# Kernel optimization log

Hardware: AMD Instinct MI355X
Metric: run time of the kernel (lower is better)

The kernel has to match this reference:

```python
import jax, jax.numpy as jnp
import numpy as np

B, S, D = 2, 2048, 512
H, DK, DV = 8, 64, 64
TEMP = DK ** 0.5


def setup_inputs() -> dict:
    key = jax.random.key(0)
    ks = jax.random.split(key, 12)
    inp = {
        "q": jax.random.normal(ks[0], (B, S, D), dtype=jnp.float32),
        "k": jax.random.normal(ks[1], (B, S, D), dtype=jnp.float32),
        "v": jax.random.normal(ks[2], (B, S, D), dtype=jnp.float32),
        "static_cov": jax.random.normal(ks[3], (B, S, S), dtype=jnp.float32),
        "mask": jax.random.randint(ks[4], (B, S, S), 0, 2, dtype=jnp.int32),
        # learned params (torch Linear(bias=False) weight is [out,in]; we store [in,out])
        "w_q": jax.random.normal(ks[5], (D, H * DK), dtype=jnp.float32) / np.sqrt(D),
        "w_k": jax.random.normal(ks[6], (D, H * DK), dtype=jnp.float32) / np.sqrt(D),
        "w_v": jax.random.normal(ks[7], (D, H * DV), dtype=jnp.float32) / np.sqrt(D),
        "w_fc": jax.random.normal(ks[8], (H * DV, D), dtype=jnp.float32) / np.sqrt(H * DV),
        "lambda_w": 10.0 * jnp.ones((1, H, 1, 1), dtype=jnp.float32),
        "ln_gamma": jnp.ones((D,), dtype=jnp.float32),
        "ln_beta": jnp.zeros((D,), dtype=jnp.float32),
    }
    return inp


def reference(q, k, v, static_cov, mask, w_q, w_k, w_v, w_fc, lambda_w, ln_gamma, ln_beta):
    residual = q
    # LayerNorm(eps=1e-6) on q only
    mu = jnp.mean(q, axis=-1, keepdims=True)
    var = jnp.mean(jnp.square(q - mu), axis=-1, keepdims=True)
    qn = (q - mu) / jnp.sqrt(var + 1e-6) * ln_gamma + ln_beta
    # projections -> [B, H, S, d]
    qh = (qn @ w_q).reshape(B, S, H, DK).transpose(0, 2, 1, 3)
    kh = (k @ w_k).reshape(B, S, H, DK).transpose(0, 2, 1, 3)
    vh = (v @ w_v).reshape(B, S, H, DV).transpose(0, 2, 1, 3)
    # convex blend of QK^T and static bias
    scores = jnp.einsum('bhqd,bhkd->bhqk', qh / TEMP, kh)  # [B,H,S,S]
    attn = scores / (lambda_w + 1.0) + (lambda_w / (lambda_w + 1.0)) * static_cov[:, None]
    attn = jnp.where(mask[:, None] == 0, -1e9, attn)
    attn = jax.nn.softmax(attn, axis=-1)
    out = jnp.einsum('bhqk,bhkd->bhqd', attn, vh)
    out = out.transpose(0, 2, 1, 3).reshape(B, S, H * DV)
    out = out @ w_fc + residual
    return (out, attn)
```

## Files before the change

### kernel.cpp

```cpp
#include <hip/hip_runtime.h>
#include <hip/hip_bf16.h>

typedef __attribute__((ext_vector_type(4))) float f32x4;
typedef __attribute__((ext_vector_type(4))) int i32x4;
typedef __attribute__((ext_vector_type(4))) unsigned int u32x4;
typedef __attribute__((ext_vector_type(8))) __bf16 bf16x8;

#define SDIM 2048
#define DDIM 512
#define HH 8
#define DH 64

static __device__ __forceinline__ f32x4 mfma_raw(bf16x8 a, bf16x8 b, f32x4 c) {
  return __builtin_amdgcn_mfma_f32_16x16x32_bf16(a, b, c, 0, 0, 0);
}

template <bool C1>
static __device__ __forceinline__ f32x4 mf(bf16x8 a, bf16x8 b, f32x4 c) {
  return C1 ? mfma_raw(a, b, c) : mfma_raw(b, a, c);
}

static __device__ __forceinline__ unsigned pack_bf16(float a, float b) {
  __bf16 x = (__bf16)a, y = (__bf16)b;
  unsigned short ux = __builtin_bit_cast(unsigned short, x);
  unsigned short uy = __builtin_bit_cast(unsigned short, y);
  return ((unsigned)uy << 16) | (unsigned)ux;
}

__global__ __launch_bounds__(256) void stageA_kernel(const float* __restrict__ cov,
                                                     const int* __restrict__ mask,
                                                     float* __restrict__ covm,
                                                     const float* __restrict__ q,
                                                     const float* __restrict__ gamma,
                                                     const float* __restrict__ beta,
                                                     __bf16* __restrict__ qn,
                                                     const float* __restrict__ w0,
                                                     const float* __restrict__ w1,
                                                     const float* __restrict__ w2,
                                                     const float* __restrict__ w3,
                                                     __bf16* __restrict__ t0,
                                                     __bf16* __restrict__ t1,
                                                     __bf16* __restrict__ t2,
                                                     __bf16* __restrict__ t3,
                                                     int* __restrict__ flag) {
  __shared__ float tile[64][65];
  int bid = blockIdx.x;
  if (bid < 8192) {
    size_t i = ((size_t)bid * 256 + threadIdx.x) * 4;
    f32x4 c = *(const f32x4*)(cov + i);
    i32x4 m = *(const i32x4*)(mask + i);
    f32x4 o;
#pragma unroll
    for (int r = 0; r < 4; ++r) o[r] = (m[r] == 0) ? -1e38f : c[r];
    *(f32x4*)(covm + i) = o;
    return;
  }
  if (bid < 9216) {
    int lb = bid - 8192;
    if (lb == 0 && threadIdx.x < 64) {
      float av = (float)(threadIdx.x & 15);
      float bv = av * av;
      bf16x8 a, b;
#pragma unroll
      for (int i = 0; i < 8; ++i) { a[i] = (__bf16)av; b[i] = (__bf16)bv; }
      f32x4 d = {};
      d = mfma_raw(a, b, d);
      if (threadIdx.x == 17) *flag = (d[0] == 128.0f) ? 1 : 2;
    }
    int row = lb * 4 + (threadIdx.x >> 6);
    int lane = threadIdx.x & 63;
    const float* qr = q + (size_t)row * DDIM + lane * 8;
    f32x4 x0 = *(const f32x4*)qr;
    f32x4 x1 = *(const f32x4*)(qr + 4);
    float s = 0.f;
#pragma unroll
    for (int i = 0; i < 4; ++i) s += x0[i] + x1[i];
#pragma unroll
    for (int off = 32; off; off >>= 1) s += __shfl_xor(s, off);
    float mu = s * (1.f / DDIM);
    float vs = 0.f;
#pragma unroll
    for (int i = 0; i < 4; ++i) {
      float d0 = x0[i] - mu, d1 = x1[i] - mu;
      vs += d0 * d0 + d1 * d1;
    }
#pragma unroll
    for (int off = 32; off; off >>= 1) vs += __shfl_xor(vs, off);
    float inv = rsqrtf(vs * (1.f / DDIM) + 1e-6f);
    const float* g = gamma + lane * 8;
    const float* be = beta + lane * 8;
    bf16x8 o;
#pragma unroll
    for (int i = 0; i < 8; ++i) {
      float xv = (i < 4) ? x0[i] : x1[i - 4];
      o[i] = (__bf16)((xv - mu) * inv * g[i] + be[i]);
    }
    *(bf16x8*)(qn + (size_t)row * DDIM + lane * 8) = o;
    return;
  }
  int wb = bid - 9216;
  int which = wb >> 6;
  int rem = wb & 63;
  int n0 = (rem & 7) * 64;
  int k0 = (rem >> 3) * 64;
  const float* w = which == 0 ? w0 : which == 1 ? w1 : which == 2 ? w2 : w3;
  __bf16* t = which == 0 ? t0 : which == 1 ? t1 : which == 2 ? t2 : t3;
  int tx = threadIdx.x & 63, ty = threadIdx.x >> 6;
#pragma unroll
  for (int j = 0; j < 16; ++j) {
    int kk = ty * 16 + j;
    tile[kk][tx] = w[(size_t)(k0 + kk) * DDIM + n0 + tx];
  }
  __syncthreads();
#pragma unroll
  for (int j = 0; j < 16; ++j) {
    int n = ty * 16 + j;
    t[(size_t)(n0 + n) * DDIM + k0 + tx] = (__bf16)tile[tx][n];
  }
}

template <bool C1>
static __device__ __forceinline__ void proj_body(const __bf16* __restrict__ qn,
                                                 const float* __restrict__ kin,
                                                 const float* __restrict__ vin,
                                                 const __bf16* __restrict__ wqT,
                                                 const __bf16* __restrict__ wkT,
                                                 const __bf16* __restrict__ wvT,
                                                 const float* __restrict__ lam,
                                                 __bf16* __restrict__ qh,
                                                 __bf16* __restrict__ kh,
                                                 __bf16* __restrict__ vT,
                                                 __bf16* __restrict__ tr) {
  int which = blockIdx.z;
  int n0 = blockIdx.x * 64;
  int m0 = blockIdx.y * 64;
  int wid = threadIdx.x >> 6, lane = threadIdx.x & 63;
  int lr = lane & 15, lg = lane >> 4;
  int mrow = m0 + wid * 16;
  const __bf16* wT = which == 0 ? wqT : which == 1 ? wkT : wvT;
  f32x4 acc[4] = {};
  for (int kb = 0; kb < DDIM; kb += 32) {
    bf16x8 afrag;
    if (which == 0) {
      afrag = *(const bf16x8*)(qn + (size_t)(mrow + lr) * DDIM + kb + lg * 8);
    } else {
      const float* src = (which == 1 ? kin : vin) + (size_t)(mrow + lr) * DDIM + kb + lg * 8;
      f32x4 y0 = *(const f32x4*)src;
      f32x4 y1 = *(const f32x4*)(src + 4);
#pragma unroll
      for (int i = 0; i < 4; ++i) { afrag[i] = (__bf16)y0[i]; afrag[i + 4] = (__bf16)y1[i]; }
    }
#pragma unroll
    for (int c = 0; c < 4; ++c) {
      bf16x8 bfrag = *(const bf16x8*)(wT + (size_t)(n0 + c * 16 + lr) * DDIM + kb + lg * 8);
      acc[c] = mf<C1>(afrag, bfrag, acc[c]);
    }
  }
  int h = n0 >> 6;
  int bq = m0 >> 11;
  int ss0 = m0 & 2047;
  if (which == 0) {
    float sc = 1.f / (8.f * (lam[h] + 1.f));
#pragma unroll
    for (int c = 0; c < 4; ++c)
#pragma unroll
      for (int r = 0; r < 4; ++r)
        tr[(wid * 16 + lg * 4 + r) * 72 + c * 16 + lr] = (__bf16)(acc[c][r] * sc);
  } else if (which == 1) {
#pragma unroll
    for (int c = 0; c < 4; ++c)
#pragma unroll
      for (int r = 0; r < 4; ++r)
        tr[(wid * 16 + lg * 4 + r) * 72 + c * 16 + lr] = (__bf16)acc[c][r];
  } else {
#pragma unroll
    for (int c = 0; c < 4; ++c)
#pragma unroll
      for (int r = 0; r < 4; ++r)
        tr[(c * 16 + lr) * 72 + wid * 16 + lg * 4 + r] = (__bf16)acc[c][r];
  }
  __syncthreads();
  size_t bh2 = (size_t)bq * HH + h;
#pragma unroll
  for (int ii = 0; ii < 2; ++ii) {
    int row = (threadIdx.x >> 3) + ii * 32;
    int col = (threadIdx.x & 7) * 8;
    bf16x8 v8 = *(const bf16x8*)(tr + row * 72 + col);
    if (which == 2) {
      *(bf16x8*)(vT + (bh2 * DH + row) * SDIM + ss0 + col) = v8;
    } else {
      __bf16* dst = (which == 0 ? qh : kh);
      *(bf16x8*)(dst + (bh2 * SDIM + ss0 + row) * DH + col) = v8;
    }
  }
}

__global__ __launch_bounds__(256) void proj_kernel(const __bf16* __restrict__ qn,
                                                   const float* __restrict__ kin,
                                                   const float* __restrict__ vin,
                                                   const __bf16* __restrict__ wqT,
                                                   const __bf16* __restrict__ wkT,
                                                   const __bf16* __restrict__ wvT,
                                                   const float* __restrict__ lam,
                                                   __bf16* __restrict__ qh,
                                                   __bf16* __restrict__ kh,
                                                   __bf16* __restrict__ vT,
                                                   const int* __restrict__ flag) {
  extern __shared__ __bf16 psm[];
  if (*flag == 1) proj_body<true>(qn, kin, vin, wqT, wkT, wvT, lam, qh, kh, vT, psm);
  else            proj_body<false>(qn, kin, vin, wqT, wkT, wvT, lam, qh, kh, vT, psm);
}

template <bool C1>
static __device__ __forceinline__ void fused_body(const __bf16* __restrict__ qh,
                                                  const __bf16* __restrict__ kh,
                                                  const __bf16* __restrict__ vT,
                                                  const float* __restrict__ covm,
                                                  const float* __restrict__ lam,
                                                  float* __restrict__ attn,
                                                  __bf16* __restrict__ oh,
                                                  float* __restrict__ smem) {
  float* part  = smem;
  float* wredm = smem + 16 * 64 * 17;
  float* wreds = wredm + 256;
  int bid = blockIdx.x;
  int xcd = bid & 7;
  int seq = bid >> 3;
  int bh  = xcd * 2 + (seq & 1);
  int q0  = (seq >> 1) * 16;
  int b = bh >> 3, h = bh & 7;
  int wid = threadIdx.x >> 6, lane = threadIdx.x & 63;
  int lr = lane & 15, lg = lane >> 4;
  int col0 = wid * 128;
  const __bf16* qbase = qh + ((size_t)bh * SDIM + q0) * DH;
  const __bf16* kbase = kh + (size_t)bh * SDIM * DH;
  bf16x8 qf0 = *(const bf16x8*)(qbase + lr * DH + lg * 8);
  bf16x8 qf1 = *(const bf16x8*)(qbase + lr * DH + 32 + lg * 8);
  f32x4 acc[8];
#pragma unroll
  for (int c = 0; c < 8; ++c) {
    const __bf16* kp = kbase + (size_t)(col0 + c * 16 + lr) * DH + lg * 8;
    bf16x8 k0 = *(const bf16x8*)kp;
    bf16x8 k1 = *(const bf16x8*)(kp + 32);
    f32x4 t = {};
    t = mf<C1>(k0, qf0, t);
    t = mf<C1>(k1, qf1, t);
    acc[c] = t;
  }
  float blend = lam[h] / (lam[h] + 1.f);
  const float* crow = covm + ((size_t)b * SDIM + q0 + lr) * SDIM + col0 + lg * 4;
  float mx = -3.4e38f;
#pragma unroll
  for (int c = 0; c < 8; ++c) {
    f32x4 cv = *(const f32x4*)(crow + c * 16);
#pragma unroll
    for (int r = 0; r < 4; ++r) {
      float valv = acc[c][r] + blend * cv[r];
      valv = (cv[r] < -1e30f) ? -1e9f : valv;
      acc[c][r] = valv;
      mx = fmaxf(mx, valv);
    }
  }
  mx = fmaxf(mx, __shfl_xor(mx, 16));
  mx = fmaxf(mx, __shfl_xor(mx, 32));
  float sm = 0.f;
#pragma unroll
  for (int c = 0; c < 8; ++c) {
#pragma unroll
    for (int r = 0; r < 4; ++r) {
      float p = __expf(acc[c][r] - mx);
      acc[c][r] = p;
      sm += p;
    }
  }
  sm += __shfl_xor(sm, 16);
  sm += __shfl_xor(sm, 32);
  if (lg == 0) {
    wredm[wid * 16 + lr] = mx;
    wreds[wid * 16 + lr] = sm;
  }
  __syncthreads();
  float M = wredm[lr];
#pragma unroll
  for (int w = 1; w < 16; ++w) M = fmaxf(M, wredm[w * 16 + lr]);
  float denom = 0.f;
#pragma unroll
  for (int w = 0; w < 16; ++w) denom += wreds[w * 16 + lr] * __expf(wredm[w * 16 + lr] - M);
  float sc = __expf(mx - M) / denom;
  unsigned pw[8][2];
#pragma unroll
  for (int c = 0; c < 8; ++c) {
    pw[c][0] = pack_bf16(acc[c][0] * sc, acc[c][1] * sc);
    pw[c][1] = pack_bf16(acc[c][2] * sc, acc[c][3] * sc);
  }
  const __bf16* vbase = vT + (size_t)bh * DH * SDIM + col0;
  int src0 = lr + 32 * (lg & 1);
  int src1 = src0 + 16;
  bool hi = (lg & 2) != 0;
  f32x4 oacc[4] = {};
#pragma unroll
  for (int t = 0; t < 4; ++t) {
    unsigned a0 = (unsigned)__shfl((int)pw[t * 2][0], src0);
    unsigned a1 = (unsigned)__shfl((int)pw[t * 2][1], src0);
    unsigned b0 = (unsigned)__shfl((int)pw[t * 2 + 1][0], src0);
    unsigned b1 = (unsigned)__shfl((int)pw[t * 2 + 1][1], src0);
    unsigned a2 = (unsigned)__shfl((int)pw[t * 2][0], src1);
    unsigned a3 = (unsigned)__shfl((int)pw[t * 2][1], src1);
    unsigned b2 = (unsigned)__shfl((int)pw[t * 2 + 1][0], src1);
    unsigned b3 = (unsigned)__shfl((int)pw[t * 2 + 1][1], src1);
    u32x4 wv;
    wv[0] = hi ? b0 : a0;
    wv[1] = hi ? b1 : a1;
    wv[2] = hi ? b2 : a2;
    wv[3] = hi ? b3 : a3;
    bf16x8 pfrag = __builtin_bit_cast(bf16x8, wv);
#pragma unroll
    for (int cp = 0; cp < 4; ++cp) {
      bf16x8 vfrag = *(const bf16x8*)(vbase + (size_t)(cp * 16 + lr) * SDIM + t * 32 + lg * 8);
      oacc[cp] = mf<C1>(vfrag, pfrag, oacc[cp]);
    }
  }
#pragma unroll
  for (int cp = 0; cp < 4; ++cp)
#pragma unroll
    for (int rp = 0; rp < 4; ++rp)
      part[(wid * 64 + cp * 16 + lg * 4 + rp) * 17 + lr] = oacc[cp][rp];
  __syncthreads();
  float* abase = attn + ((size_t)bh * SDIM + q0 + lr) * SDIM + col0 + lg * 4;
#pragma unroll
  for (int c = 0; c < 8; ++c) {
    f32x4 pn;
#pragma unroll
    for (int r = 0; r < 4; ++r) pn[r] = acc[c][r] * sc;
    *(f32x4*)(abase + c * 16) = pn;
  }
  {
    int qq = threadIdx.x >> 6;
    int dv = threadIdx.x & 63;
    float s = 0.f;
#pragma unroll
    for (int w = 0; w < 16; ++w) s += part[(w * 64 + dv) * 17 + qq];
    float sn = __shfl_xor(s, 1);
    if ((dv & 1) == 0) {
      unsigned ow = pack_bf16(s, sn);
      *(unsigned*)(oh + ((size_t)(b * SDIM + q0 + qq)) * DDIM + h * DH + dv) = ow;
    }
  }
}

__global__ __launch_bounds__(1024, 4) void fused_kernel_cov(const __bf16* __restrict__ qh,
                                                            const __bf16* __restrict__ kh,
                                                            const __bf16* __restrict__ vT,
                                                            const float* __restrict__ covm,
                                                            const float* __restrict__ lam,
                                                            float* __restrict__ attn,
                                                            __bf16* __restrict__ oh,
                                                            const int* __restrict__ flag) {
  extern __shared__ float smem[];
  if (*flag == 1) fused_body<true>(qh, kh, vT, covm, lam, attn, oh, smem);
  else            fused_body<false>(qh, kh, vT, covm, lam, attn, oh, smem);
}

template <bool C1>
static __device__ __forceinline__ void fc_body(const __bf16* __restrict__ oh,
                                               const __bf16* __restrict__ wfcT,
                                               const float* __restrict__ resid,
                                               float* __restrict__ out) {
  int n0 = blockIdx.x * 64;
  int m0 = blockIdx.y * 64;
  int wid = threadIdx.x >> 6, lane = threadIdx.x & 63;
  int lr = lane & 15, lg = lane >> 4;
  int mrow = m0 + wid * 16;
  f32x4 acc[4] = {};
  for (int kb = 0; kb < DDIM; kb += 32) {
    bf16x8 afrag = *(const bf16x8*)(oh + (size_t)(mrow + lr) * DDIM + kb + lg * 8);
#pragma unroll
    for (int c = 0; c < 4; ++c) {
      bf16x8 bfrag = *(const bf16x8*)(wfcT + (size_t)(n0 + c * 16 + lr) * DDIM + kb + lg * 8);
      acc[c] = mf<C1>(afrag, bfrag, acc[c]);
    }
  }
#pragma unroll
  for (int c = 0; c < 4; ++c)
#pragma unroll
    for (int r = 0; r < 4; ++r) {
      size_t m = mrow + lg * 4 + r;
      size_t n = n0 + c * 16 + lr;
      out[m * DDIM + n] = acc[c][r] + resid[m * DDIM + n];
    }
}

__global__ __launch_bounds__(256) void fc_kernel(const __bf16* __restrict__ oh,
                                                 const __bf16* __restrict__ wfcT,
                                                 const float* __restrict__ resid,
                                                 float* __restrict__ out,
                                                 const int* __restrict__ flag) {
  if (*flag == 1) fc_body<true>(oh, wfcT, resid, out);
  else            fc_body<false>(oh, wfcT, resid, out);
}

extern "C" void kernel_launch(void* const* d_in, const int* in_sizes, int n_in,
                              void* d_out, int out_size, void* d_ws, size_t ws_size,
                              hipStream_t stream) {
  const float* q = (const float*)d_in[0];
  const float* k = (const float*)d_in[1];
  const float* v = (const float*)d_in[2];
  const float* static_cov = (const float*)d_in[3];
  const int* mask = (const int*)d_in[4];
  const float* w_q = (const float*)d_in[5];
  const float* w_k = (const float*)d_in[6];
  const float* w_v = (const float*)d_in[7];
  const float* w_fc = (const float*)d_in[8];
  const float* lam = (const float*)d_in[9];
  const float* gamma = (const float*)d_in[10];
  const float* beta = (const float*)d_in[11];

  float* out = (float*)d_out;
  float* attn = out + (size_t)2 * SDIM * DDIM;

  char* ws = (char*)d_ws;
  const size_t MB4 = (size_t)4 << 20;
  __bf16* qn  = (__bf16*)(ws);
  __bf16* qh  = (__bf16*)(ws + 1 * MB4);
  __bf16* kh  = (__bf16*)(ws + 2 * MB4);
  __bf16* vT  = (__bf16*)(ws + 3 * MB4);
  __bf16* oh  = (__bf16*)(ws + 4 * MB4);
  __bf16* wqT = (__bf16*)(ws + 5 * MB4);
  __bf16* wkT = (__bf16*)(ws + 5 * MB4 + 524288);
  __bf16* wvT = (__bf16*)(ws + 5 * MB4 + 2 * 524288);
  __bf16* wfcT= (__bf16*)(ws + 5 * MB4 + 3 * 524288);
  int* flag   = (int*)(ws + 5 * MB4 + 4 * 524288);
  float* covm = (float*)(ws + 6 * MB4);

  const unsigned fused_smem = (16 * 64 * 17 + 256 + 256) * 4;
  const unsigned proj_smem  = 64 * 72 * 2;

  stageA_kernel<<<dim3(9472), dim3(256), 0, stream>>>(static_cov, mask, covm,
                                                      q, gamma, beta, qn,
                                                      w_q, w_k, w_v, w_fc,
                                                      wqT, wkT, wvT, wfcT, flag);
  proj_kernel<<<dim3(8, 64, 3), dim3(256), proj_smem, stream>>>(qn, k, v, wqT, wkT, wvT, lam, qh, kh, vT, flag);
  fused_kernel_cov<<<dim3(2048), dim3(1024), fused_smem, stream>>>(qh, kh, vT, covm, lam, attn, oh, flag);
  fc_kernel<<<dim3(8, 64), dim3(256), 0, stream>>>(oh, wfcT, q, out, flag);
}
```

Baseline: 311.5 us.

## Halve fused attention block to 8 waves, each covering 256 key columns

The fused attention kernel now launches 512 threads per block instead of 1024, and each wave handles 256 key columns (16 MFMA tiles) instead of 128. Fewer waves shrink the cross-wave max/sum reduction and the shared-memory partial PV buffer. The softmax normalisation scale is no longer applied to the probabilities before packing them to bf16; it is applied to the PV accumulator afterwards. The cost is higher register pressure per thread (acc[16]) and less thread-level parallelism per block.

```diff
diff --git a/kernel.cpp b/kernel.cpp
--- a/kernel.cpp
+++ b/kernel.cpp
@@ -221,8 +221,8 @@
                                                   __bf16* __restrict__ oh,
                                                   float* __restrict__ smem) {
   float* part  = smem;
-  float* wredm = smem + 16 * 64 * 17;
-  float* wreds = wredm + 256;
+  float* wredm = smem + 8 * 64 * 17;
+  float* wreds = wredm + 128;
   int bid = blockIdx.x;
   int xcd = bid & 7;
   int seq = bid >> 3;
@@ -231,14 +231,14 @@
   int b = bh >> 3, h = bh & 7;
   int wid = threadIdx.x >> 6, lane = threadIdx.x & 63;
   int lr = lane & 15, lg = lane >> 4;
-  int col0 = wid * 128;
+  int col0 = wid * 256;
   const __bf16* qbase = qh + ((size_t)bh * SDIM + q0) * DH;
   const __bf16* kbase = kh + (size_t)bh * SDIM * DH;
   bf16x8 qf0 = *(const bf16x8*)(qbase + lr * DH + lg * 8);
   bf16x8 qf1 = *(const bf16x8*)(qbase + lr * DH + 32 + lg * 8);
-  f32x4 acc[8];
-#pragma unroll
-  for (int c = 0; c < 8; ++c) {
+  f32x4 acc[16];
+#pragma unroll
+  for (int c = 0; c < 16; ++c) {
     const __bf16* kp = kbase + (size_t)(col0 + c * 16 + lr) * DH + lg * 8;
     bf16x8 k0 = *(const bf16x8*)kp;
     bf16x8 k1 = *(const bf16x8*)(kp + 32);
@@ -251,7 +251,7 @@
   const float* crow = covm + ((size_t)b * SDIM + q0 + lr) * SDIM + col0 + lg * 4;
   float mx = -3.4e38f;
 #pragma unroll
-  for (int c = 0; c < 8; ++c) {
+  for (int c = 0; c < 16; ++c) {
     f32x4 cv = *(const f32x4*)(crow + c * 16);
 #pragma unroll
     for (int r = 0; r < 4; ++r) {
@@ -265,7 +265,7 @@
   mx = fmaxf(mx, __shfl_xor(mx, 32));
   float sm = 0.f;
 #pragma unroll
-  for (int c = 0; c < 8; ++c) {
+  for (int c = 0; c < 16; ++c) {
 #pragma unroll
     for (int r = 0; r < 4; ++r) {
       float p = __expf(acc[c][r] - mx);
@@ -282,32 +282,30 @@
   __syncthreads();
   float M = wredm[lr];
 #pragma unroll
-  for (int w = 1; w < 16; ++w) M = fmaxf(M, wredm[w * 16 + lr]);
+  for (int w = 1; w < 8; ++w) M = fmaxf(M, wredm[w * 16 + lr]);
   float denom = 0.f;
 #pragma unroll
-  for (int w = 0; w < 16; ++w) denom += wreds[w * 16 + lr] * __expf(wredm[w * 16 + lr] - M);
+  for (int w = 0; w < 8; ++w) denom += wreds[w * 16 + lr] * __expf(wredm[w * 16 + lr] - M);
   float sc = __expf(mx - M) / denom;
-  unsigned pw[8][2];
-#pragma unroll
-  for (int c = 0; c < 8; ++c) {
-    pw[c][0] = pack_bf16(acc[c][0] * sc, acc[c][1] * sc);
-    pw[c][1] = pack_bf16(acc[c][2] * sc, acc[c][3] * sc);
-  }
   const __bf16* vbase = vT + (size_t)bh * DH * SDIM + col0;
   int src0 = lr + 32 * (lg & 1);
   int src1 = src0 + 16;
   bool hi = (lg & 2) != 0;
   f32x4 oacc[4] = {};
 #pragma unroll
-  for (int t = 0; t < 4; ++t) {
-    unsigned a0 = (unsigned)__shfl((int)pw[t * 2][0], src0);
-    unsigned a1 = (unsigned)__shfl((int)pw[t * 2][1], src0);
-    unsigned b0 = (unsigned)__shfl((int)pw[t * 2 + 1][0], src0);
-    unsigned b1 = (unsigned)__shfl((int)pw[t * 2 + 1][1], src0);
-    unsigned a2 = (unsigned)__shfl((int)pw[t * 2][0], src1);
-    unsigned a3 = (unsigned)__shfl((int)pw[t * 2][1], src1);
-    unsigned b2 = (unsigned)__shfl((int)pw[t * 2 + 1][0], src1);
-    unsigned b3 = (unsigned)__shfl((int)pw[t * 2 + 1][1], src1);
+  for (int t = 0; t < 8; ++t) {
+    unsigned p0 = pack_bf16(acc[t * 2][0], acc[t * 2][1]);
+    unsigned p1 = pack_bf16(acc[t * 2][2], acc[t * 2][3]);
+    unsigned p2 = pack_bf16(acc[t * 2 + 1][0], acc[t * 2 + 1][1]);
+    unsigned p3 = pack_bf16(acc[t * 2 + 1][2], acc[t * 2 + 1][3]);
+    unsigned a0 = (unsigned)__shfl((int)p0, src0);
+    unsigned a1 = (unsigned)__shfl((int)p1, src0);
+    unsigned b0 = (unsigned)__shfl((int)p2, src0);
+    unsigned b1 = (unsigned)__shfl((int)p3, src0);
+    unsigned a2 = (unsigned)__shfl((int)p0, src1);
+    unsigned a3 = (unsigned)__shfl((int)p1, src1);
+    unsigned b2 = (unsigned)__shfl((int)p2, src1);
+    unsigned b3 = (unsigned)__shfl((int)p3, src1);
     u32x4 wv;
     wv[0] = hi ? b0 : a0;
     wv[1] = hi ? b1 : a1;
@@ -324,38 +322,38 @@
   for (int cp = 0; cp < 4; ++cp)
 #pragma unroll
     for (int rp = 0; rp < 4; ++rp)
-      part[(wid * 64 + cp * 16 + lg * 4 + rp) * 17 + lr] = oacc[cp][rp];
+      part[(wid * 64 + cp * 16 + lg * 4 + rp) * 17 + lr] = oacc[cp][rp] * sc;
   __syncthreads();
   float* abase = attn + ((size_t)bh * SDIM + q0 + lr) * SDIM + col0 + lg * 4;
 #pragma unroll
-  for (int c = 0; c < 8; ++c) {
+  for (int c = 0; c < 16; ++c) {
     f32x4 pn;
 #pragma unroll
     for (int r = 0; r < 4; ++r) pn[r] = acc[c][r] * sc;
     *(f32x4*)(abase + c * 16) = pn;
   }
   {
-    int qq = threadIdx.x >> 6;
-    int dv = threadIdx.x & 63;
-    float s = 0.f;
-#pragma unroll
-    for (int w = 0; w < 16; ++w) s += part[(w * 64 + dv) * 17 + qq];
-    float sn = __shfl_xor(s, 1);
-    if ((dv & 1) == 0) {
-      unsigned ow = pack_bf16(s, sn);
-      *(unsigned*)(oh + ((size_t)(b * SDIM + q0 + qq)) * DDIM + h * DH + dv) = ow;
-    }
-  }
-}
-
-__global__ __launch_bounds__(1024, 4) void fused_kernel_cov(const __bf16* __restrict__ qh,
-                                                            const __bf16* __restrict__ kh,
-                                                            const __bf16* __restrict__ vT,
-                                                            const float* __restrict__ covm,
-                                                            const float* __restrict__ lam,
-                                                            float* __restrict__ attn,
-                                                            __bf16* __restrict__ oh,
-                                                            const int* __restrict__ flag) {
+    int qq = threadIdx.x >> 5;
+    int dv = (threadIdx.x & 31) * 2;
+    float s0 = 0.f, s1 = 0.f;
+#pragma unroll
+    for (int w = 0; w < 8; ++w) {
+      s0 += part[(w * 64 + dv) * 17 + qq];
+      s1 += part[(w * 64 + dv + 1) * 17 + qq];
+    }
+    unsigned ow = pack_bf16(s0, s1);
+    *(unsigned*)(oh + ((size_t)(b * SDIM + q0 + qq)) * DDIM + h * DH + dv) = ow;
+  }
+}
+
+__global__ __launch_bounds__(512, 4) void fused_kernel_cov(const __bf16* __restrict__ qh,
+                                                           const __bf16* __restrict__ kh,
+                                                           const __bf16* __restrict__ vT,
+                                                           const float* __restrict__ covm,
+                                                           const float* __restrict__ lam,
+                                                           float* __restrict__ attn,
+                                                           __bf16* __restrict__ oh,
+                                                           const int* __restrict__ flag) {
   extern __shared__ float smem[];
   if (*flag == 1) fused_body<true>(qh, kh, vT, covm, lam, attn, oh, smem);
   else            fused_body<false>(qh, kh, vT, covm, lam, attn, oh, smem);
@@ -432,7 +430,7 @@
   int* flag   = (int*)(ws + 5 * MB4 + 4 * 524288);
   float* covm = (float*)(ws + 6 * MB4);
 
-  const unsigned fused_smem = (16 * 64 * 17 + 256 + 256) * 4;
+  const unsigned fused_smem = (8 * 64 * 17 + 128 + 128) * 4;
   const unsigned proj_smem  = 64 * 72 * 2;
 
   stageA_kernel<<<dim3(9472), dim3(256), 0, stream>>>(static_cov, mask, covm,
@@ -440,6 +438,6 @@
                                                       w_q, w_k, w_v, w_fc,
                                                       wqT, wkT, wvT, wfcT, flag);
   proj_kernel<<<dim3(8, 64, 3), dim3(256), proj_smem, stream>>>(qn, k, v, wqT, wkT, wvT, lam, qh, kh, vT, flag);
-  fused_kernel_cov<<<dim3(2048), dim3(1024), fused_smem, stream>>>(qh, kh, vT, covm, lam, attn, oh, flag);
+  fused_kernel_cov<<<dim3(2048), dim3(512), fused_smem, stream>>>(qh, kh, vT, covm, lam, attn, oh, flag);
   fc_kernel<<<dim3(8, 64), dim3(256), 0, stream>>>(oh, wfcT, q, out, flag);
 }
```

Result: faster. 299.9 us (-3.7%).
